# Kernel tuning notes

Hardware: AMD Instinct MI355X
Metric: run time of the kernel (lower is better)

## Reference

```python
import jax, jax.numpy as jnp
import numpy as np

NN_SIZE = 16
RADIUS2 = 0.5 * 0.5  # radius^2
EPS = 0.0001


def setup_inputs() -> dict:
    key = jax.random.key(0)
    points = jax.random.normal(key, (4, 8192, 3), dtype=jnp.float32)
    return {"points": points}


def reference(points):
    # points: (B, N, 3)
    B, N, C = points.shape
    # Brute-force KNN (pytorch3d ops.knn_points with K = nn_size + 1, self included)
    sq = jnp.sum(points * points, axis=-1)  # (B, N)
    d2_all = sq[:, :, None] + sq[:, None, :] - 2.0 * jnp.einsum('bnc,bmc->bnm', points, points)  # (B,N,N)
    _, idx = jax.lax.top_k(-d2_all, NN_SIZE + 1)  # smallest distances first, (B,N,K+1)
    knn_idx = idx[:, :, 1:]  # drop self, (B, N, K)
    # Gather neighbor coordinates; detached in the original (.detach())
    knn_points = jax.vmap(lambda p, i: p[i])(points, knn_idx)  # (B, N, K, 3)
    knn_points = jax.lax.stop_gradient(knn_points)
    # Recompute squared distances (as the module does)
    knn_v = knn_points - points[:, :, None, :]  # (B, N, K, 3)
    distance2 = jnp.sum(knn_v * knn_v, axis=-1)  # (B, N, K)
    loss = 1.0 / jnp.sqrt(distance2 + EPS)
    loss = jnp.where(distance2 < RADIUS2, loss, jnp.zeros_like(loss))
    # reduction == 'mean'
    return jnp.mean(loss)
```

## Files before the change

### kernel.cpp

```cpp
#include <hip/hip_runtime.h>

#define NPTS 8192
#define NBATCH 4
#define NTOT (NBATCH * NPTS)
#define NN 16
#define RAD2 0.25f
#define EPSF 1e-4f
#define BIGF 1e30f

#define GC 16
#define GP 18
#define CBS 6144
#define NCELL_TOT (NBATCH * CBS)

#define STHR 256
#define SWV 4
#define PPW 2
#define SNB (NTOT / (SWV * PPW))
#define HCAP 384

#define LOG2C 5.0103f
#define NCLAMP 257

#define WS_COUNTS 0
#define WS_RANGES (WS_COUNTS + NCELL_TOT * 4)
#define WS_CURSOR (WS_RANGES + NCELL_TOT * 8)
#define WS_SORTED (WS_CURSOR + NCELL_TOT * 4)
#define WS_BSUMS  (WS_SORTED + (NTOT + 64) * 16)
#define WS_NEEDED (WS_BSUMS + SNB * 4)

__device__ __forceinline__ int cellc(float v) {
  return min(max((int)floorf((v + 4.0f) * 2.0f), 0), GC - 1);
}

__device__ __forceinline__ float prsqrt(float x) {
  float r = __builtin_amdgcn_rsqf(x);
  r = r * fmaf(-0.5f * x * r, r, 1.5f);
  return r;
}

#define CE(a, b) { const float lo_ = fminf(a, b); const float hi_ = fmaxf(a, b); a = lo_; b = hi_; }


__global__ __launch_bounds__(256)
void hist_kernel(const float* __restrict__ pts, int* __restrict__ counts) {
  const int i = blockIdx.x * 256 + threadIdx.x;
  if (i >= NTOT) return;
  const int b = i >> 13;
  const float x = pts[i * 3 + 0], y = pts[i * 3 + 1], z = pts[i * 3 + 2];
  const int c = b * CBS + ((cellc(z) + 1) * GP + (cellc(y) + 1)) * GP + (cellc(x) + 1);
  atomicAdd(&counts[c], 1);
}

__global__ __launch_bounds__(1024)
void scan_kernel(const int* __restrict__ counts, int2* __restrict__ ranges,
                 int* __restrict__ cursor) {
  __shared__ int wtot[16];
  __shared__ int woff[16];
  const int b = blockIdx.x;
  const int tid = threadIdx.x;
  const int wid = tid >> 6;
  const int lane = tid & 63;
  const int g0 = b * CBS + tid * 6;

  int v[6];
  int lsum = 0;
#pragma unroll
  for (int k = 0; k < 6; ++k) { v[k] = counts[g0 + k]; lsum += v[k]; }

  int x = lsum;
  for (int off = 1; off < 64; off <<= 1) {
    const int t = __shfl_up(x, off, 64);
    if (lane >= off) x += t;
  }
  if (lane == 63) wtot[wid] = x;
  __syncthreads();
  if (wid == 0 && lane < 16) {
    int s = wtot[lane];
    for (int off = 1; off < 16; off <<= 1) {
      const int t = __shfl_up(s, off, 64);
      if (lane >= off) s += t;
    }
    woff[lane] = s - wtot[lane];
  }
  __syncthreads();

  int run = b * NPTS + woff[wid] + (x - lsum);
#pragma unroll
  for (int k = 0; k < 6; ++k) {
    ranges[g0 + k] = make_int2(run, v[k]);
    cursor[g0 + k] = run;
    run += v[k];
  }
}

__global__ __launch_bounds__(256)
void scatter_kernel(const float* __restrict__ pts, int* __restrict__ cursor,
                    float4* __restrict__ sorted) {
  const int i = blockIdx.x * 256 + threadIdx.x;
  if (i >= NTOT) return;
  const int b = i >> 13;
  const float x = pts[i * 3 + 0], y = pts[i * 3 + 1], z = pts[i * 3 + 2];
  const int c = b * CBS + ((cellc(z) + 1) * GP + (cellc(y) + 1)) * GP + (cellc(x) + 1);
  const int pos = atomicAdd(&cursor[c], 1);
  sorted[pos] = make_float4(x, y, z, fmaf(x, x, fmaf(y, y, z * z)));
}


__device__ __forceinline__ int scan1(const float4* __restrict__ sorted,
    const int* rs, const int* re, float rr, int selfp,
    float m2x, float m2y, float m2z, float sp, float* __restrict__ hq, int lane) {
  int hcnt = 0;
  const unsigned long long below = (1ull << lane) - 1ull;
#pragma unroll
  for (int m = 0; m < 9; ++m) {
    const int s = rs[m], e = re[m];
    for (int j0 = s; j0 < e; j0 += 64) {
      const int j = j0 + lane;
      float d2 = BIGF;
      if (j < e) {
        const float4 q = sorted[j];
        d2 = fmaf(q.x, m2x, fmaf(q.y, m2y, fmaf(q.z, m2z, q.w + sp)));
      }
      const bool hit = (d2 < rr) && (j != selfp);
      const unsigned long long bal = __ballot(hit);
      if (bal) {
        const int pos = hcnt + (int)__popcll(bal & below);
        if (hit && pos < HCAP) hq[pos] = d2;
        hcnt += (int)__popcll(bal);
      }
    }
  }
  return hcnt;
}

__device__ __forceinline__ void scan2(const float4* __restrict__ sorted,
    const int* rs, const int* re, float rr,
    int pA, float m2xA, float m2yA, float m2zA, float spA,
    int pB, float m2xB, float m2yB, float m2zB, float spB,
    float* __restrict__ hqA, float* __restrict__ hqB, int lane,
    int& hcntA, int& hcntB) {
  int hA = 0, hB = 0;
  const unsigned long long below = (1ull << lane) - 1ull;
#pragma unroll
  for (int m = 0; m < 9; ++m) {
    const int s = rs[m], e = re[m];
    for (int j0 = s; j0 < e; j0 += 64) {
      const int j = j0 + lane;
      float d2A = BIGF, d2B = BIGF;
      if (j < e) {
        const float4 q = sorted[j];
        const float qw = q.w;
        d2A = fmaf(q.x, m2xA, fmaf(q.y, m2yA, fmaf(q.z, m2zA, qw + spA)));
        d2B = fmaf(q.x, m2xB, fmaf(q.y, m2yB, fmaf(q.z, m2zB, qw + spB)));
      }
      const bool hitA = (d2A < rr) && (j != pA);
      const unsigned long long balA = __ballot(hitA);
      if (balA) {
        const int posA = hA + (int)__popcll(balA & below);
        if (hitA && posA < HCAP) hqA[posA] = d2A;
        hA += (int)__popcll(balA);
      }
      const bool hitB = (d2B < rr) && (j != pB);
      const unsigned long long balB = __ballot(hitB);
      if (balB) {
        const int posB = hB + (int)__popcll(balB & below);
        if (hitB && posB < HCAP) hqB[posB] = d2B;
        hB += (int)__popcll(balB);
      }
    }
  }
  hcntA = hA;
  hcntB = hB;
}

template<int R>
__device__ __forceinline__ float tourney(const float* __restrict__ hq, int hn, int lane) {
  float v[R];
#pragma unroll
  for (int r = 0; r < R; ++r) {
    const int idx = lane + 64 * r;
    v[r] = (idx < hn) ? hq[idx] : BIGF;
  }
  if constexpr (R == 3) { CE(v[0], v[1]); CE(v[1], v[2]); CE(v[0], v[1]); }
  if constexpr (R == 6) {
    CE(v[0], v[1]); CE(v[2], v[3]); CE(v[4], v[5]);
    CE(v[1], v[2]); CE(v[3], v[4]);
    CE(v[0], v[1]); CE(v[2], v[3]); CE(v[4], v[5]);
    CE(v[1], v[2]); CE(v[3], v[4]);
    CE(v[0], v[1]); CE(v[2], v[3]); CE(v[4], v[5]);
    CE(v[1], v[2]); CE(v[3], v[4]);
  }
  float loss = 0.0f;
#pragma unroll
  for (int r = 0; r < NN; ++r) {
    float g = v[0];
    g = fminf(g, __shfl_xor(g, 1));
    g = fminf(g, __shfl_xor(g, 2));
    g = fminf(g, __shfl_xor(g, 4));
    g = fminf(g, __shfl_xor(g, 8));
    g = fminf(g, __shfl_xor(g, 16));
    g = fminf(g, __shfl_xor(g, 32));
    loss += prsqrt(g + EPSF);
    const unsigned long long own = __ballot(v[0] == g);
    const int first = (int)(__ffsll((unsigned long long)own) - 1);
    if (lane == first) {
#pragma unroll
      for (int r2 = 0; r2 < R - 1; ++r2) v[r2] = v[r2 + 1];
      v[R - 1] = BIGF;
    }
  }
  return loss;
}

__device__ __forceinline__ float extract_loss(const float* __restrict__ hq, int hn, int lane) {
  if (hn <= NN) {
    float l = (lane < hn) ? prsqrt(hq[lane] + EPSF) : 0.0f;
    l += __shfl_xor(l, 1);
    l += __shfl_xor(l, 2);
    l += __shfl_xor(l, 4);
    l += __shfl_xor(l, 8);
    l += __shfl_xor(l, 16);
    l += __shfl_xor(l, 32);
    return l;
  }
  if (hn <= 64) {
    float v = (lane < hn) ? hq[lane] : BIGF;
#pragma unroll
    for (int k = 2; k <= 64; k <<= 1) {
#pragma unroll
      for (int j = k >> 1; j > 0; j >>= 1) {
        const float o = __shfl_xor(v, j, 64);
        const bool keepmin = (((lane & j) == 0) != ((lane & k) != 0));
        v = keepmin ? fminf(v, o) : fmaxf(v, o);
      }
    }
    float l = (lane < NN && v < RAD2) ? prsqrt(v + EPSF) : 0.0f;
    l += __shfl_xor(l, 1);
    l += __shfl_xor(l, 2);
    l += __shfl_xor(l, 4);
    l += __shfl_xor(l, 8);
    l += __shfl_xor(l, 16);
    l += __shfl_xor(l, 32);
    return l;
  } else if (hn <= 192) {
    return tourney<3>(hq, hn, lane);
  }
  return tourney<6>(hq, hn, lane);
}


__global__ __launch_bounds__(STHR)
void search_kernel(const float4* __restrict__ sorted, const int2* __restrict__ rngs,
                   float* __restrict__ bsums) {
  __shared__ float hbuf[SWV][2][HCAP];
  __shared__ float wloss[SWV];

  const int tid = threadIdx.x;
  const int wv = tid >> 6;
  const int lane = tid & 63;
  const int pair = wv * SNB + blockIdx.x;
  const int p0 = pair * 2;
  const int p1 = p0 + 1;
  const int bb = p0 >> 13;

  const float4 ptA = sorted[p0];
  const float4 ptB = sorted[p1];
  const float m2xA = -2.0f * ptA.x, m2yA = -2.0f * ptA.y, m2zA = -2.0f * ptA.z;
  const float spA = ptA.w;
  const float m2xB = -2.0f * ptB.x, m2yB = -2.0f * ptB.y, m2zB = -2.0f * ptB.z;
  const float spB = ptB.w;

  const int rbA = __builtin_amdgcn_readfirstlane(
      bb * CBS + ((cellc(ptA.z) + 1) * GP + (cellc(ptA.y) + 1)) * GP);
  const int rbB = __builtin_amdgcn_readfirstlane(
      bb * CBS + ((cellc(ptB.z) + 1) * GP + (cellc(ptB.y) + 1)) * GP);
  const int xA = __builtin_amdgcn_readfirstlane(cellc(ptA.x));
  const int xB = __builtin_amdgcn_readfirstlane(cellc(ptB.x));

  const int rowoff[9] = {
    (-1 * GP - 1) * GP, (-1 * GP + 0) * GP, (-1 * GP + 1) * GP,
    ( 0 * GP - 1) * GP, ( 0 * GP + 0) * GP, ( 0 * GP + 1) * GP,
    ( 1 * GP - 1) * GP, ( 1 * GP + 0) * GP, ( 1 * GP + 1) * GP };

  float* hqA = hbuf[wv][0];
  float* hqB = hbuf[wv][1];
  int hnA, hnB;

  if (rbA == rbB) {
    const int lo = min(xA, xB);
    const int hi = max(xA, xB) + 2;
    int rs[9], re[9], ncand = 0;
#pragma unroll
    for (int m = 0; m < 9; ++m) {
      const int base = rbA + rowoff[m];
      const int2 a = rngs[base + lo];
      const int2 b = rngs[base + hi];
      rs[m] = a.x;
      re[m] = b.x + b.y;
      ncand += re[m] - rs[m];
    }
    const bool clamped = (ncand <= NCLAMP);
    float r0sq = RAD2;
    if (!clamped) r0sq = exp2f((LOG2C - log2f((float)ncand)) * (2.0f / 3.0f));

    int hA, hB;
    scan2(sorted, rs, re, r0sq, p0, m2xA, m2yA, m2zA, spA,
          p1, m2xB, m2yB, m2zB, spB, hqA, hqB, lane, hA, hB);
    hnA = min(hA, HCAP);
    hnB = min(hB, HCAP);
    if (hnA < NN && !clamped)
      hnA = min(scan1(sorted, rs, re, RAD2, p0, m2xA, m2yA, m2zA, spA, hqA, lane), HCAP);
    if (hnB < NN && !clamped)
      hnB = min(scan1(sorted, rs, re, RAD2, p1, m2xB, m2yB, m2zB, spB, hqB, lane), HCAP);
  } else {
    int rsA[9], reA[9], ncA = 0, rsB[9], reB[9], ncB = 0;
#pragma unroll
    for (int m = 0; m < 9; ++m) {
      const int baseA = rbA + rowoff[m];
      const int2 a0 = rngs[baseA + xA];
      const int2 a1 = rngs[baseA + xA + 2];
      rsA[m] = a0.x; reA[m] = a1.x + a1.y; ncA += reA[m] - rsA[m];
      const int baseB = rbB + rowoff[m];
      const int2 b0 = rngs[baseB + xB];
      const int2 b1 = rngs[baseB + xB + 2];
      rsB[m] = b0.x; reB[m] = b1.x + b1.y; ncB += reB[m] - rsB[m];
    }
    const bool clA = (ncA <= NCLAMP);
    const bool clB = (ncB <= NCLAMP);
    float rA = RAD2, rB = RAD2;
    if (!clA) rA = exp2f((LOG2C - log2f((float)ncA)) * (2.0f / 3.0f));
    if (!clB) rB = exp2f((LOG2C - log2f((float)ncB)) * (2.0f / 3.0f));
    hnA = min(scan1(sorted, rsA, reA, rA, p0, m2xA, m2yA, m2zA, spA, hqA, lane), HCAP);
    if (hnA < NN && !clA)
      hnA = min(scan1(sorted, rsA, reA, RAD2, p0, m2xA, m2yA, m2zA, spA, hqA, lane), HCAP);
    hnB = min(scan1(sorted, rsB, reB, rB, p1, m2xB, m2yB, m2zB, spB, hqB, lane), HCAP);
    if (hnB < NN && !clB)
      hnB = min(scan1(sorted, rsB, reB, RAD2, p1, m2xB, m2yB, m2zB, spB, hqB, lane), HCAP);
  }

  const float lossA = extract_loss(hqA, hnA, lane);
  const float lossB = extract_loss(hqB, hnB, lane);

  if (lane == 0) wloss[wv] = lossA + lossB;
  __syncthreads();
  if (tid == 0) {
    float s = 0.0f;
#pragma unroll
    for (int w = 0; w < SWV; ++w) s += wloss[w];
    bsums[blockIdx.x] = s;
  }
}

__global__ __launch_bounds__(256)
void finalize_kernel(const float* __restrict__ block_sums, int nblocks,
                     float* __restrict__ out) {
  __shared__ float s[256];
  float v = 0.0f;
  for (int idx = threadIdx.x; idx < nblocks; idx += 256) v += block_sums[idx];
  s[threadIdx.x] = v;
  __syncthreads();
  for (int off = 128; off > 0; off >>= 1) {
    if (threadIdx.x < off) s[threadIdx.x] += s[threadIdx.x + off];
    __syncthreads();
  }
  if (threadIdx.x == 0) out[0] = s[0] / (float)(NBATCH * NPTS * NN);
}


#define DTILE 1024
#define DNT 512
#define DNW 8
#define DNB (NTOT / 64)
#define CSTRIDE 17
#define QTRIG 13

__device__ __forceinline__ void insert16(float (&td)[NN], float& thrmax, float v) {
  if (v < thrmax) {
    bool done = false;
#pragma unroll
    for (int k = 0; k < NN; ++k) {
      const bool hit = (!done) && (td[k] == thrmax);
      if (hit) td[k] = v;
      done = done || hit;
    }
    thrmax = td[0];
#pragma unroll
    for (int k = 1; k < NN; ++k) thrmax = fmaxf(thrmax, td[k]);
  }
}

__device__ __forceinline__ void drain_queue(float* buf, int qbase, int& cnt,
                                            float (&td)[NN], float& thrmax) {
#pragma unroll
  for (int c = 0; c < 16; ++c) {
    const float v = (c < cnt) ? buf[qbase + c] : BIGF;
    insert16(td, thrmax, v);
  }
  cnt = 0;
}

__global__ __launch_bounds__(DNT)
void dense_kernel(const float* __restrict__ pts, float* __restrict__ block_sums) {
  __shared__ float4 tile[DTILE];
  __shared__ float buf[DNT * CSTRIDE];

  const int tid = threadIdx.x;
  const int wave = tid >> 6;
  const int lane = tid & 63;
  const int bid = blockIdx.x;
  const int b = bid / (NPTS / 64);
  const int base = (bid % (NPTS / 64)) * 64;
  const float* __restrict__ bp = pts + (size_t)b * NPTS * 3;

  const int i = base + lane;
  const float xi = bp[i * 3 + 0];
  const float yi = bp[i * 3 + 1];
  const float zi = bp[i * 3 + 2];

  float td[NN];
#pragma unroll
  for (int k = 0; k < NN; ++k) td[k] = BIGF;
  float thrmax = BIGF;
  int cnt = 0;
  const int qbase = tid * CSTRIDE;

  for (int tb = 0; tb < NPTS; tb += DTILE) {
    for (int pp = tid; pp < DTILE; pp += DNT) {
      const float* sp = bp + (size_t)(tb + pp) * 3;
      tile[pp] = make_float4(sp[0], sp[1], sp[2], 0.0f);
    }
    __syncthreads();
    const int jb = wave * (DTILE / DNW);
    for (int jj = 0; jj < DTILE / DNW; ++jj) {
      const float4 q = tile[jb + jj];
      const float ddx = q.x - xi, ddy = q.y - yi, ddz = q.z - zi;
      const float d2 = fmaf(ddx, ddx, fmaf(ddy, ddy, ddz * ddz));
      if (d2 < RAD2 && d2 != 0.0f) {
        buf[qbase + cnt] = d2;
        ++cnt;
      }
      if (__any(cnt >= QTRIG)) drain_queue(buf, qbase, cnt, td, thrmax);
    }
    __syncthreads();
  }
  drain_queue(buf, qbase, cnt, td, thrmax);
#pragma unroll
  for (int k = 0; k < NN; ++k) buf[qbase + k] = td[k];
  __syncthreads();

  if (wave == 0) {
    float sd[NN];
#pragma unroll
    for (int k = 0; k < NN; ++k) sd[k] = BIGF;
    float smax = BIGF;
    for (int w = 0; w < DNW; ++w) {
      for (int c = 0; c < NN; ++c) {
        insert16(sd, smax, buf[(w * 64 + lane) * CSTRIDE + c]);
      }
    }
    float loss = 0.0f;
#pragma unroll
    for (int k = 0; k < NN; ++k) {
      if (sd[k] < RAD2) loss += 1.0f / sqrtf(sd[k] + EPSF);
    }
    for (int off = 32; off > 0; off >>= 1) loss += __shfl_down(loss, off);
    if (lane == 0) block_sums[bid] = loss;
  }
}


extern "C" void kernel_launch(void* const* d_in, const int* in_sizes, int n_in,
                              void* d_out, int out_size, void* d_ws, size_t ws_size,
                              hipStream_t stream) {
  const float* pts = (const float*)d_in[0];
  float* out = (float*)d_out;
  char* ws = (char*)d_ws;

  if (ws_size >= (size_t)WS_NEEDED) {
    int* counts = (int*)(ws + WS_COUNTS);
    int2* rngs = (int2*)(ws + WS_RANGES);
    int* cursor = (int*)(ws + WS_CURSOR);
    float4* sorted = (float4*)(ws + WS_SORTED);
    float* bsums = (float*)(ws + WS_BSUMS);

    hipMemsetAsync(counts, 0, NCELL_TOT * 4, stream);
    hist_kernel<<<(NTOT + 255) / 256, 256, 0, stream>>>(pts, counts);
    scan_kernel<<<NBATCH, 1024, 0, stream>>>(counts, rngs, cursor);
    scatter_kernel<<<(NTOT + 255) / 256, 256, 0, stream>>>(pts, cursor, sorted);
    search_kernel<<<SNB, STHR, 0, stream>>>(sorted, rngs, bsums);
    finalize_kernel<<<1, 256, 0, stream>>>(bsums, SNB, out);
  } else {
    float* bsums = (float*)ws;
    dense_kernel<<<DNB, DNT, 0, stream>>>(pts, bsums);
    finalize_kernel<<<1, 256, 0, stream>>>(bsums, DNB, out);
  }
}
```

Baseline: 58.84 us.

## Fold finalize into search via last-block reduction and vectorize hist/scatter loads

The final reduction moves into the search kernel: each block publishes its partial sum with release semantics and bumps an atomic done counter, and the last block to finish sums all partials and writes the mean. This removes one kernel launch and its launch gap. The histogram and scatter kernels now have each thread load three float4s covering four points, cutting the thread count fourfold and using wider loads. This relies on the done counter being zeroed by the extended memset and on correct memory ordering. Scatter order within cells also changes, and with it the order of sorted points.

```diff
diff --git a/kernel.cpp b/kernel.cpp
--- a/kernel.cpp
+++ b/kernel.cpp
@@ -23,7 +23,8 @@
 #define NCLAMP 257
 
 #define WS_COUNTS 0
-#define WS_RANGES (WS_COUNTS + NCELL_TOT * 4)
+#define WS_DONE   (WS_COUNTS + NCELL_TOT * 4)
+#define WS_RANGES (WS_DONE + 16)
 #define WS_CURSOR (WS_RANGES + NCELL_TOT * 8)
 #define WS_SORTED (WS_CURSOR + NCELL_TOT * 4)
 #define WS_BSUMS  (WS_SORTED + (NTOT + 64) * 16)
@@ -43,13 +44,18 @@
 
 
 __global__ __launch_bounds__(256)
-void hist_kernel(const float* __restrict__ pts, int* __restrict__ counts) {
-  const int i = blockIdx.x * 256 + threadIdx.x;
-  if (i >= NTOT) return;
-  const int b = i >> 13;
-  const float x = pts[i * 3 + 0], y = pts[i * 3 + 1], z = pts[i * 3 + 2];
-  const int c = b * CBS + ((cellc(z) + 1) * GP + (cellc(y) + 1)) * GP + (cellc(x) + 1);
-  atomicAdd(&counts[c], 1);
+void hist_kernel(const float4* __restrict__ pts4, int* __restrict__ counts) {
+  const int t = blockIdx.x * 256 + threadIdx.x;
+  if (t >= NTOT / 4) return;
+  const float4 f0 = pts4[t * 3 + 0];
+  const float4 f1 = pts4[t * 3 + 1];
+  const float4 f2 = pts4[t * 3 + 2];
+  const int b = (t * 4) >> 13;
+  const int base = b * CBS;
+  atomicAdd(&counts[base + ((cellc(f0.z) + 1) * GP + (cellc(f0.y) + 1)) * GP + (cellc(f0.x) + 1)], 1);
+  atomicAdd(&counts[base + ((cellc(f1.y) + 1) * GP + (cellc(f1.x) + 1)) * GP + (cellc(f0.w) + 1)], 1);
+  atomicAdd(&counts[base + ((cellc(f2.x) + 1) * GP + (cellc(f1.w) + 1)) * GP + (cellc(f1.z) + 1)], 1);
+  atomicAdd(&counts[base + ((cellc(f2.w) + 1) * GP + (cellc(f2.z) + 1)) * GP + (cellc(f2.y) + 1)], 1);
 }
 
 __global__ __launch_bounds__(1024)
@@ -95,15 +101,25 @@
 }
 
 __global__ __launch_bounds__(256)
-void scatter_kernel(const float* __restrict__ pts, int* __restrict__ cursor,
+void scatter_kernel(const float4* __restrict__ pts4, int* __restrict__ cursor,
                     float4* __restrict__ sorted) {
-  const int i = blockIdx.x * 256 + threadIdx.x;
-  if (i >= NTOT) return;
-  const int b = i >> 13;
-  const float x = pts[i * 3 + 0], y = pts[i * 3 + 1], z = pts[i * 3 + 2];
-  const int c = b * CBS + ((cellc(z) + 1) * GP + (cellc(y) + 1)) * GP + (cellc(x) + 1);
-  const int pos = atomicAdd(&cursor[c], 1);
-  sorted[pos] = make_float4(x, y, z, fmaf(x, x, fmaf(y, y, z * z)));
+  const int t = blockIdx.x * 256 + threadIdx.x;
+  if (t >= NTOT / 4) return;
+  const float4 f0 = pts4[t * 3 + 0];
+  const float4 f1 = pts4[t * 3 + 1];
+  const float4 f2 = pts4[t * 3 + 2];
+  const int b = (t * 4) >> 13;
+  const int base = b * CBS;
+  float px[4] = { f0.x, f0.w, f1.z, f2.y };
+  float py[4] = { f0.y, f1.x, f1.w, f2.z };
+  float pz[4] = { f0.z, f1.y, f2.x, f2.w };
+#pragma unroll
+  for (int k = 0; k < 4; ++k) {
+    const int c = base + ((cellc(pz[k]) + 1) * GP + (cellc(py[k]) + 1)) * GP + (cellc(px[k]) + 1);
+    const int pos = atomicAdd(&cursor[c], 1);
+    sorted[pos] = make_float4(px[k], py[k], pz[k],
+                              fmaf(px[k], px[k], fmaf(py[k], py[k], pz[k] * pz[k])));
+  }
 }
 
 
@@ -252,9 +268,11 @@
 
 __global__ __launch_bounds__(STHR)
 void search_kernel(const float4* __restrict__ sorted, const int2* __restrict__ rngs,
-                   float* __restrict__ bsums) {
+                   float* __restrict__ bsums, int* __restrict__ done,
+                   float* __restrict__ out) {
   __shared__ float hbuf[SWV][2][HCAP];
   __shared__ float wloss[SWV];
+  __shared__ int lastflag;
 
   const int tid = threadIdx.x;
   const int wv = tid >> 6;
@@ -348,7 +366,24 @@
     float s = 0.0f;
 #pragma unroll
     for (int w = 0; w < SWV; ++w) s += wloss[w];
-    bsums[blockIdx.x] = s;
+    __hip_atomic_store(&bsums[blockIdx.x], s, __ATOMIC_RELEASE, __HIP_MEMORY_SCOPE_AGENT);
+    const int d = __hip_atomic_fetch_add(done, 1, __ATOMIC_ACQ_REL, __HIP_MEMORY_SCOPE_AGENT);
+    lastflag = (d == SNB - 1);
+  }
+  __syncthreads();
+
+  if (lastflag) {
+    float v = 0.0f;
+    for (int idx = tid; idx < SNB; idx += STHR)
+      v += __hip_atomic_load(&bsums[idx], __ATOMIC_RELAXED, __HIP_MEMORY_SCOPE_AGENT);
+    __shared__ float s2[STHR];
+    s2[tid] = v;
+    __syncthreads();
+    for (int off = STHR / 2; off > 0; off >>= 1) {
+      if (tid < off) s2[tid] += s2[tid + off];
+      __syncthreads();
+    }
+    if (tid == 0) out[0] = s2[0] / (float)(NBATCH * NPTS * NN);
   }
 }
 
@@ -479,17 +514,17 @@
 
   if (ws_size >= (size_t)WS_NEEDED) {
     int* counts = (int*)(ws + WS_COUNTS);
+    int* done = (int*)(ws + WS_DONE);
     int2* rngs = (int2*)(ws + WS_RANGES);
     int* cursor = (int*)(ws + WS_CURSOR);
     float4* sorted = (float4*)(ws + WS_SORTED);
     float* bsums = (float*)(ws + WS_BSUMS);
 
-    hipMemsetAsync(counts, 0, NCELL_TOT * 4, stream);
-    hist_kernel<<<(NTOT + 255) / 256, 256, 0, stream>>>(pts, counts);
+    hipMemsetAsync(counts, 0, NCELL_TOT * 4 + 16, stream);
+    hist_kernel<<<(NTOT / 4 + 255) / 256, 256, 0, stream>>>((const float4*)pts, counts);
     scan_kernel<<<NBATCH, 1024, 0, stream>>>(counts, rngs, cursor);
-    scatter_kernel<<<(NTOT + 255) / 256, 256, 0, stream>>>(pts, cursor, sorted);
-    search_kernel<<<SNB, STHR, 0, stream>>>(sorted, rngs, bsums);
-    finalize_kernel<<<1, 256, 0, stream>>>(bsums, SNB, out);
+    scatter_kernel<<<(NTOT / 4 + 255) / 256, 256, 0, stream>>>((const float4*)pts, cursor, sorted);
+    search_kernel<<<SNB, STHR, 0, stream>>>(sorted, rngs, bsums, done, out);
   } else {
     float* bsums = (float*)ws;
     dense_kernel<<<DNB, DNT, 0, stream>>>(pts, bsums);
```

New measurement: 148.4 us. +152.2%, slower.
